# Kernel tuning notes

Hardware: AMD Instinct MI355X
Metric: run time of the kernel (lower is better)

Reference implementation:

```python
import jax, jax.numpy as jnp
import numpy as np

S = 1024          # tokens (prefill)
DIM = 2560
HEAD_DIM = 128
N_HEADS = 20
N_KV = 5
HPG = N_HEADS // N_KV      # heads per kv group = 4
GS = 128                   # weight-scale group size
THETA = 500000.0
EPS = 1e-05
QKV_OUT = (N_HEADS + 2 * N_KV) * HEAD_DIM  # 3840


def setup_inputs() -> dict:
    key = jax.random.key(0)
    ks = jax.random.split(key, 7)
    x = jax.random.normal(ks[0], (S, DIM), jnp.float32)
    # unpacked int2 (ternary) weights, stored as float for the reference math
    w_qkv = jax.random.randint(ks[1], (QKV_OUT, DIM), -1, 2).astype(jnp.float32)
    ws_qkv = jax.random.uniform(ks[2], (QKV_OUT, DIM // GS), jnp.float32, 0.01, 0.05)
    w_o = jax.random.randint(ks[3], (DIM, N_HEADS * HEAD_DIM), -1, 2).astype(jnp.float32)
    ws_o = jax.random.uniform(ks[4], (DIM, N_HEADS * HEAD_DIM // GS), jnp.float32, 0.01, 0.05)
    q_norm_w = 1.0 + 0.02 * jax.random.normal(ks[5], (HEAD_DIM,), jnp.float32)
    k_norm_w = 1.0 + 0.02 * jax.random.normal(ks[6], (HEAD_DIM,), jnp.float32)
    return {"x": x, "w_qkv": w_qkv, "ws_qkv": ws_qkv, "w_o": w_o, "ws_o": ws_o,
            "q_norm_w": q_norm_w, "k_norm_w": k_norm_w}


def _quant_act(x):
    # per-token symmetric int8 quant: s = 127 / max|x| (clamped)
    s = 127.0 / jnp.clip(jnp.max(jnp.abs(x), axis=-1, keepdims=True), 1e-05, None)
    q = jnp.clip(jnp.round(x * s), -128.0, 127.0)
    return q, s


def _bitlinear(x, w, ws):
    # int8 activation x int2 weight GEMM with per-(out,group) dequant scales
    q, s = _quant_act(x)
    w_dq = w * jnp.repeat(ws, GS, axis=1)        # [out, in]
    return (q @ w_dq.T) / s


def _rmsnorm(x, w):
    return x * jax.lax.rsqrt(jnp.mean(x * x, axis=-1, keepdims=True) + EPS) * w


def _rope(x, cos, sin):
    # x: [S, ..., d]; cos/sin: [S, d//2], interleaved-pair (llama) convention
    d2 = x.shape[-1] // 2
    shape = (x.shape[0],) + (1,) * (x.ndim - 2) + (d2,)
    c = cos.reshape(shape)
    s = sin.reshape(shape)
    xr = x.reshape(x.shape[:-1] + (d2, 2))
    x0, x1 = xr[..., 0], xr[..., 1]
    out = jnp.stack([x0 * c - x1 * s, x0 * s + x1 * c], axis=-1)
    return out.reshape(x.shape)


def reference(x, w_qkv, ws_qkv, w_o, ws_o, q_norm_w, k_norm_w):
    qkv = _bitlinear(x, w_qkv, ws_qkv)                       # [S, 3840]
    q_size = N_HEADS * HEAD_DIM
    k_size = N_KV * HEAD_DIM
    xq = qkv[:, :q_size].reshape(S, N_KV, HPG, HEAD_DIM)     # [S, g, h, d]
    xk = qkv[:, q_size:q_size + k_size].reshape(S, N_KV, HEAD_DIM)
    xv = qkv[:, q_size + k_size:].reshape(S, N_KV, HEAD_DIM)
    xq = _rmsnorm(xq, q_norm_w)
    xk = _rmsnorm(xk, k_norm_w)
    # RoPE (prefill: positions 0..S-1)
    pos = jnp.arange(S, dtype=jnp.float32)
    inv_freq = THETA ** (-jnp.arange(0, HEAD_DIM, 2, dtype=jnp.float32) / HEAD_DIM)
    ang = pos[:, None] * inv_freq[None, :]                   # [S, d/2]
    cos, sin = jnp.cos(ang), jnp.sin(ang)
    xq = _rope(xq, cos, sin)
    xk = _rope(xk, cos, sin)
    # GQA causal flash-attention math
    scale = HEAD_DIM ** -0.5
    scores = jnp.einsum('sghd,tgd->ghst', xq, xk) * scale    # [g, h, S, S]
    causal = jnp.tril(jnp.ones((S, S), bool))
    scores = jnp.where(causal, scores, -1e30)
    attn = jax.nn.softmax(scores, axis=-1)
    out = jnp.einsum('ghst,tgd->sghd', attn, xv).reshape(S, N_HEADS * HEAD_DIM)
    return _bitlinear(out, w_o, ws_o)                        # [S, DIM]
```

## Files before the change

### kernel.cpp

```cpp
#include <hip/hip_runtime.h>
#include <hip/hip_bf16.h>
#include <cstdint>
#include <math.h>

#define SEQ 1024
#define DIM 2560
#define HD 128
#define NH 20
#define NKV 5
#define QKV_OUT 3840
#define GS 128

typedef __bf16 bf16;
typedef __bf16 bf16x4 __attribute__((ext_vector_type(4)));
typedef __bf16 bf16x8 __attribute__((ext_vector_type(8)));
typedef float f32x4 __attribute__((ext_vector_type(4)));

template <typename T>
__global__ __launch_bounds__(256) void quant_kernel(
    const T* __restrict__ x, bf16* __restrict__ act,
    float* __restrict__ rs, int cols) {
  const int row = blockIdx.x;
  const int tid = threadIdx.x;
  const T* xr = x + (size_t)row * cols;
  float m = 0.f;
  for (int i = tid; i < cols; i += 256) m = fmaxf(m, fabsf((float)xr[i]));
  for (int off = 32; off; off >>= 1) m = fmaxf(m, __shfl_xor(m, off));
  __shared__ float red[4];
  __shared__ float s_bc;
  if ((tid & 63) == 0) red[tid >> 6] = m;
  __syncthreads();
  if (tid == 0) {
    float mm = fmaxf(fmaxf(red[0], red[1]), fmaxf(red[2], red[3]));
    mm = fmaxf(mm, 1e-5f);
    s_bc = 127.f / mm;
    rs[row] = mm / 127.f;
  }
  __syncthreads();
  const float s = s_bc;
  bf16* ar = act + (size_t)row * cols;
  for (int i = tid; i < cols; i += 256) {
    float q = rintf((float)xr[i] * s);
    q = fminf(fmaxf(q, -128.f), 127.f);
    ar[i] = (bf16)q;
  }
}

__global__ __launch_bounds__(256) void dequant2_kernel(
    const float* __restrict__ w1, const float* __restrict__ ws1, bf16* __restrict__ o1,
    const float* __restrict__ w2, const float* __restrict__ ws2, bf16* __restrict__ o2,
    long n1_4, long total4) {
  long i = (long)blockIdx.x * 256 + threadIdx.x;
  if (i >= total4) return;
  const float* w; const float* ws; bf16* o; long e;
  if (i < n1_4) { w = w1; ws = ws1; o = o1; e = i * 4; }
  else          { w = w2; ws = ws2; o = o2; e = (i - n1_4) * 4; }
  int row = (int)(e / DIM);
  int k = (int)(e % DIM);
  float sc = ws[(size_t)row * (DIM / GS) + (k / GS)];
  float4 wv = *(const float4*)(w + e);
  bf16x4 ov;
  ov[0] = (bf16)(wv.x * sc);
  ov[1] = (bf16)(wv.y * sc);
  ov[2] = (bf16)(wv.z * sc);
  ov[3] = (bf16)(wv.w * sc);
  *(bf16x4*)(o + e) = ov;
}

__device__ __forceinline__ void gload_lds16(const bf16* g, bf16* l) {
  __builtin_amdgcn_global_load_lds(
      (const __attribute__((address_space(1))) void*)g,
      (__attribute__((address_space(3))) void*)l, 16, 0, 0);
}

__global__ __launch_bounds__(256) void gemm_bt(
    const bf16* __restrict__ A, const bf16* __restrict__ B,
    const float* __restrict__ rs, float* __restrict__ C,
    int N, int K, int Kh, size_t part_stride) {
  __shared__ bf16 As[64 * 64];
  __shared__ bf16 Bs[128 * 64];
  const int tid = threadIdx.x;
  const int w = tid >> 6, l = tid & 63;
  const int row0 = blockIdx.y * 64;
  const int col0 = blockIdx.x * 128;
  const int z = blockIdx.z;
  const int wm = (w >> 1) * 32, wn = (w & 1) * 64;
  const int lcol = l & 15, quad = l >> 4;
  const int sr = l >> 3;
  const int sg = l & 7;
  const bf16* Ag = A + (size_t)row0 * K + (size_t)z * Kh;
  const bf16* Bg = B + (size_t)col0 * K + (size_t)z * Kh;

  f32x4 acc[2][4] = {};

  for (int k0 = 0; k0 < Kh; k0 += 64) {
    __syncthreads();
#pragma unroll
    for (int i = 0; i < 2; ++i) {
      int rb = w * 16 + i * 8;
      int r = rb + sr;
      gload_lds16(Ag + (size_t)r * K + k0 + ((sg ^ (r & 7)) * 8), As + rb * 64);
    }
#pragma unroll
    for (int i = 0; i < 4; ++i) {
      int rb = w * 32 + i * 8;
      int r = rb + sr;
      gload_lds16(Bg + (size_t)r * K + k0 + ((sg ^ (r & 7)) * 8), Bs + rb * 64);
    }
    __syncthreads();
#pragma unroll
    for (int ks = 0; ks < 2; ++ks) {
      bf16x8 af[2], bff[4];
#pragma unroll
      for (int mi = 0; mi < 2; ++mi) {
        int R = wm + mi * 16 + lcol;
        af[mi] = *(const bf16x8*)(As + R * 64 + (((ks * 4 + quad) ^ (R & 7)) * 8));
      }
#pragma unroll
      for (int ni = 0; ni < 4; ++ni) {
        int R = wn + ni * 16 + lcol;
        bff[ni] = *(const bf16x8*)(Bs + R * 64 + (((ks * 4 + quad) ^ (R & 7)) * 8));
      }
#pragma unroll
      for (int mi = 0; mi < 2; ++mi)
#pragma unroll
        for (int ni = 0; ni < 4; ++ni)
          acc[mi][ni] = __builtin_amdgcn_mfma_f32_16x16x32_bf16(
              af[mi], bff[ni], acc[mi][ni], 0, 0, 0);
    }
  }
  float* Cp = C + (size_t)z * part_stride;
#pragma unroll
  for (int mi = 0; mi < 2; ++mi) {
#pragma unroll
    for (int ni = 0; ni < 4; ++ni) {
      int col = col0 + wn + ni * 16 + lcol;
#pragma unroll
      for (int r = 0; r < 4; ++r) {
        int row = row0 + wm + mi * 16 + quad * 4 + r;
        Cp[(size_t)row * N + col] = acc[mi][ni][r] * rs[row];
      }
    }
  }
}

__global__ __launch_bounds__(256) void gemm_bt64(
    const bf16* __restrict__ A, const bf16* __restrict__ B,
    const float* __restrict__ rs, float* __restrict__ C, int N, int K) {
  __shared__ bf16 As[64 * 64];
  __shared__ bf16 Bs[64 * 64];
  const int tid = threadIdx.x;
  const int w = tid >> 6, l = tid & 63;
  const int row0 = blockIdx.y * 64;
  const int col0 = blockIdx.x * 64;
  const int wm = (w >> 1) * 32, wn = (w & 1) * 32;
  const int lcol = l & 15, quad = l >> 4;
  const int sr = l >> 3;
  const int sg = l & 7;
  const bf16* Ag = A + (size_t)row0 * K;
  const bf16* Bg = B + (size_t)col0 * K;

  f32x4 acc[2][2] = {};

  for (int k0 = 0; k0 < K; k0 += 64) {
    __syncthreads();
#pragma unroll
    for (int i = 0; i < 2; ++i) {
      int rb = w * 16 + i * 8;
      int r = rb + sr;
      gload_lds16(Ag + (size_t)r * K + k0 + ((sg ^ (r & 7)) * 8), As + rb * 64);
    }
#pragma unroll
    for (int i = 0; i < 2; ++i) {
      int rb = w * 16 + i * 8;
      int r = rb + sr;
      gload_lds16(Bg + (size_t)r * K + k0 + ((sg ^ (r & 7)) * 8), Bs + rb * 64);
    }
    __syncthreads();
#pragma unroll
    for (int ks = 0; ks < 2; ++ks) {
      bf16x8 af[2], bff[2];
#pragma unroll
      for (int mi = 0; mi < 2; ++mi) {
        int R = wm + mi * 16 + lcol;
        af[mi] = *(const bf16x8*)(As + R * 64 + (((ks * 4 + quad) ^ (R & 7)) * 8));
      }
#pragma unroll
      for (int ni = 0; ni < 2; ++ni) {
        int R = wn + ni * 16 + lcol;
        bff[ni] = *(const bf16x8*)(Bs + R * 64 + (((ks * 4 + quad) ^ (R & 7)) * 8));
      }
#pragma unroll
      for (int mi = 0; mi < 2; ++mi)
#pragma unroll
        for (int ni = 0; ni < 2; ++ni)
          acc[mi][ni] = __builtin_amdgcn_mfma_f32_16x16x32_bf16(
              af[mi], bff[ni], acc[mi][ni], 0, 0, 0);
    }
  }
#pragma unroll
  for (int mi = 0; mi < 2; ++mi) {
#pragma unroll
    for (int ni = 0; ni < 2; ++ni) {
      int col = col0 + wn + ni * 16 + lcol;
#pragma unroll
      for (int r = 0; r < 4; ++r) {
        int row = row0 + wm + mi * 16 + quad * 4 + r;
        C[(size_t)row * N + col] = acc[mi][ni][r] * rs[row];
      }
    }
  }
}

__global__ void qk_post(const float* __restrict__ qkvA, const float* __restrict__ qkvB,
                        const float* __restrict__ qw, const float* __restrict__ kw,
                        bf16* __restrict__ Qo, bf16* __restrict__ Ko) {
  const int t = blockIdx.x, h = blockIdx.y, i = threadIdx.x;
  const size_t off = (h < NH)
      ? (size_t)t * QKV_OUT + h * HD
      : (size_t)t * QKV_OUT + 2560 + (h - NH) * HD;
  const float* s1 = qkvA + off;
  const float* s2 = qkvB + off;
  float x0 = s1[2 * i] + s2[2 * i];
  float x1 = s1[2 * i + 1] + s2[2 * i + 1];
  float ss = x0 * x0 + x1 * x1;
  for (int off2 = 1; off2 < 64; off2 <<= 1) ss += __shfl_xor(ss, off2);
  float r = rsqrtf(ss * (1.f / 128.f) + 1e-5f);
  const float* wv = (h < NH) ? qw : kw;
  float y0 = x0 * r * wv[2 * i];
  float y1 = x1 * r * wv[2 * i + 1];
  float inv_freq = powf(500000.f, -(float)(2 * i) * (1.f / 128.f));
  float ang = (float)t * inv_freq;
  float sn, cs;
  sincosf(ang, &sn, &cs);
  float o0 = y0 * cs - y1 * sn;
  float o1 = y0 * sn + y1 * cs;
  if (h < NH) {
    bf16* dst = Qo + ((size_t)t * NH + h) * HD + 2 * i;
    dst[0] = (bf16)o0; dst[1] = (bf16)o1;
  } else {
    bf16* dst = Ko + ((size_t)(h - NH) * SEQ + t) * HD + 2 * i;
    dst[0] = (bf16)o0; dst[1] = (bf16)o1;
  }
}

__global__ __launch_bounds__(256) void v_post(const float* __restrict__ qkvA,
                                              const float* __restrict__ qkvB,
                                              bf16* __restrict__ Vt) {
  const int t0 = blockIdx.x * 64, g = blockIdx.y;
  const int tid = threadIdx.x;
  __shared__ bf16 Ls[64 * 137];
  {
    const int tl = tid >> 4;
    const int d0 = (tid & 15) * 8;
#pragma unroll
    for (int pass = 0; pass < 4; ++pass) {
      int t = pass * 16 + tl;
      size_t off = (size_t)(t0 + t) * QKV_OUT + 3200 + g * HD + d0;
      float4 a = *(const float4*)(qkvA + off);
      float4 b = *(const float4*)(qkvA + off + 4);
      float4 a2 = *(const float4*)(qkvB + off);
      float4 b2 = *(const float4*)(qkvB + off + 4);
      bf16* dst = Ls + t * 137 + d0;
      dst[0] = (bf16)(a.x + a2.x); dst[1] = (bf16)(a.y + a2.y);
      dst[2] = (bf16)(a.z + a2.z); dst[3] = (bf16)(a.w + a2.w);
      dst[4] = (bf16)(b.x + b2.x); dst[5] = (bf16)(b.y + b2.y);
      dst[6] = (bf16)(b.z + b2.z); dst[7] = (bf16)(b.w + b2.w);
    }
  }
  __syncthreads();
  {
    const int dl = tid >> 3;
    const int tl0 = (tid & 7) * 8;
#pragma unroll
    for (int pass = 0; pass < 4; ++pass) {
      int d = pass * 32 + dl;
      bf16x8 v;
#pragma unroll
      for (int j = 0; j < 8; ++j) v[j] = Ls[(tl0 + j) * 137 + d];
      *(bf16x8*)(Vt + ((size_t)g * HD + d) * SEQ + t0 + tl0) = v;
    }
  }
}

__global__ __launch_bounds__(256) void attn_mfma(
    const bf16* __restrict__ Qb, const bf16* __restrict__ Kb,
    const bf16* __restrict__ Vt, bf16* __restrict__ O) {
  const int qb = 31 - (int)blockIdx.x;
  const int hp = blockIdx.y;
  const int tid = threadIdx.x;
  const int wave = tid >> 6, lane = tid & 63;
  const int H = (hp >> 1) * 4 + (hp & 1) * 2 + (wave >> 1);
  const int g = H >> 2;
  const int qcol = lane & 15, quad = lane >> 4;
  const int q_tok = qb * 32 + (wave & 1) * 16 + qcol;
  const float scale = 0.08838834764831843f;

  __shared__ bf16 Ks[2][64 * 128];
  __shared__ bf16 Vs[2][128 * 64];

  const bf16* kbase = Kb + (size_t)g * SEQ * HD;
  const bf16* vbase = Vt + (size_t)g * HD * SEQ;

  bf16x8 qf[4];
  {
    const bf16* qp = Qb + ((size_t)q_tok * NH + H) * HD + quad * 8;
#pragma unroll
    for (int kc = 0; kc < 4; ++kc) qf[kc] = *(const bf16x8*)(qp + kc * 32);
  }

  float m_i = -1e30f, l_i = 0.f;
  f32x4 o_acc[8] = {};
  const int kt_max = (qb * 32 + 31) >> 6;

  const int k_r = lane >> 4, k_g = lane & 15;
  const int v_r = lane >> 3, v_g = lane & 7;

#define STAGE(buf, key0)                                                       \
  {                                                                            \
    _Pragma("unroll") for (int p = 0; p < 4; ++p) {                            \
      int r0 = wave * 16 + p * 4;                                              \
      int r = r0 + k_r;                                                        \
      gload_lds16(kbase + (size_t)((key0) + r) * HD + ((k_g ^ (r & 15)) * 8),  \
                  &Ks[buf][r0 * 128]);                                         \
    }                                                                          \
    _Pragma("unroll") for (int p = 0; p < 4; ++p) {                            \
      int r0 = wave * 32 + p * 8;                                              \
      int r = r0 + v_r;                                                        \
      gload_lds16(vbase + (size_t)r * SEQ + (key0) + ((v_g ^ (r & 7)) * 8),    \
                  &Vs[buf][r0 * 64]);                                          \
    }                                                                          \
  }

  STAGE(0, 0)

  for (int kt = 0; kt <= kt_max; ++kt) {
    const int key0 = kt * 64;
    __syncthreads();
    if (kt < kt_max) STAGE((kt + 1) & 1, key0 + 64)
    const bf16* Kt = Ks[kt & 1];
    const bf16* Vtile = Vs[kt & 1];

    f32x4 s[4];
#pragma unroll
    for (int mg = 0; mg < 4; ++mg) {
      const int R = mg * 16 + qcol;
      const bf16* krow = Kt + R * 128;
      f32x4 acc = {0.f, 0.f, 0.f, 0.f};
#pragma unroll
      for (int kc = 0; kc < 4; ++kc) {
        int j = kc * 4 + quad;
        bf16x8 kf = *(const bf16x8*)(krow + ((j ^ (R & 15)) * 8));
        acc = __builtin_amdgcn_mfma_f32_16x16x32_bf16(kf, qf[kc], acc, 0, 0, 0);
      }
      s[mg] = acc;
    }

    float mt = -1e30f;
#pragma unroll
    for (int mg = 0; mg < 4; ++mg)
#pragma unroll
      for (int r = 0; r < 4; ++r) {
        int key = key0 + mg * 16 + quad * 4 + r;
        float v = (key <= q_tok) ? s[mg][r] * scale : -1e30f;
        s[mg][r] = v;
        mt = fmaxf(mt, v);
      }
    mt = fmaxf(mt, __shfl_xor(mt, 16));
    mt = fmaxf(mt, __shfl_xor(mt, 32));
    float mnew = fmaxf(m_i, mt);
    float alpha = __expf(m_i - mnew);
    float ps = 0.f;
#pragma unroll
    for (int mg = 0; mg < 4; ++mg)
#pragma unroll
      for (int r = 0; r < 4; ++r) {
        float pv = __expf(s[mg][r] - mnew);
        s[mg][r] = pv;
        ps += pv;
      }
    ps += __shfl_xor(ps, 16);
    ps += __shfl_xor(ps, 32);
    l_i = l_i * alpha + ps;
    m_i = mnew;
#pragma unroll
    for (int mg2 = 0; mg2 < 8; ++mg2)
#pragma unroll
      for (int r = 0; r < 4; ++r) o_acc[mg2][r] *= alpha;

    bf16x8 pb[2];
#pragma unroll
    for (int c = 0; c < 2; ++c)
#pragma unroll
      for (int j = 0; j < 8; ++j)
        pb[c][j] = (bf16)s[c * 2 + (j >> 2)][j & 3];

#pragma unroll
    for (int mg2 = 0; mg2 < 8; ++mg2) {
      const int R = mg2 * 16 + qcol;
      const bf16* vrow = Vtile + R * 64;
      f32x4 acc = o_acc[mg2];
#pragma unroll
      for (int c = 0; c < 2; ++c) {
        int g8a = c * 8 + quad;
        int g8b = c * 8 + 4 + quad;
        bf16x4 v0 = *(const bf16x4*)(vrow + ((g8a >> 1) ^ (R & 7)) * 8 + (g8a & 1) * 4);
        bf16x4 v1 = *(const bf16x4*)(vrow + ((g8b >> 1) ^ (R & 7)) * 8 + (g8b & 1) * 4);
        bf16x8 vfr;
#pragma unroll
        for (int j = 0; j < 4; ++j) { vfr[j] = v0[j]; vfr[j + 4] = v1[j]; }
        acc = __builtin_amdgcn_mfma_f32_16x16x32_bf16(vfr, pb[c], acc, 0, 0, 0);
      }
      o_acc[mg2] = acc;
    }
  }
#undef STAGE

  const float inv = 1.f / l_i;
  bf16* op = O + (size_t)q_tok * DIM + H * HD + quad * 4;
#pragma unroll
  for (int mg2 = 0; mg2 < 8; ++mg2) {
    bf16x4 vv;
    vv[0] = (bf16)(o_acc[mg2][0] * inv);
    vv[1] = (bf16)(o_acc[mg2][1] * inv);
    vv[2] = (bf16)(o_acc[mg2][2] * inv);
    vv[3] = (bf16)(o_acc[mg2][3] * inv);
    *(bf16x4*)(op + mg2 * 16) = vv;
  }
}

extern "C" void kernel_launch(void* const* d_in, const int* in_sizes, int n_in,
                              void* d_out, int out_size, void* d_ws, size_t ws_size,
                              hipStream_t stream) {
  const float* x      = (const float*)d_in[0];
  const float* w_qkv  = (const float*)d_in[1];
  const float* ws_qkv = (const float*)d_in[2];
  const float* w_o    = (const float*)d_in[3];
  const float* ws_o   = (const float*)d_in[4];
  const float* qnw    = (const float*)d_in[5];
  const float* knw    = (const float*)d_in[6];
  float* out = (float*)d_out;

  char* p = (char*)d_ws;
  bf16*  act1 = (bf16*)p;  p += (size_t)SEQ * DIM * 2;
  float* rs1  = (float*)p; p += 4096;
  bf16*  wqdq = (bf16*)p;  p += (size_t)QKV_OUT * DIM * 2;
  bf16*  wodq = (bf16*)p;  p += (size_t)DIM * DIM * 2;
  float* qkvA = (float*)p; p += (size_t)SEQ * QKV_OUT * 4;
  float* qkvB = (float*)p; p += (size_t)SEQ * QKV_OUT * 4;
  bf16*  Qb   = (bf16*)p;  p += (size_t)SEQ * NH * HD * 2;
  bf16*  Kb   = (bf16*)p;  p += (size_t)NKV * SEQ * HD * 2;
  bf16*  Vt   = (bf16*)p;  p += (size_t)NKV * HD * SEQ * 2;
  bf16*  attn = (bf16*)p;  p += (size_t)SEQ * DIM * 2;
  bf16*  act2 = (bf16*)p;  p += (size_t)SEQ * DIM * 2;
  float* rs2  = (float*)p; p += 4096;

  quant_kernel<float><<<SEQ, 256, 0, stream>>>(x, act1, rs1, DIM);
  {
    long n1_4 = (long)QKV_OUT * DIM / 4;
    long total4 = n1_4 + (long)DIM * DIM / 4;
    dequant2_kernel<<<(int)((total4 + 255) / 256), 256, 0, stream>>>(
        w_qkv, ws_qkv, wqdq, w_o, ws_o, wodq, n1_4, total4);
  }
  gemm_bt<<<dim3(QKV_OUT / 128, SEQ / 64, 2), 256, 0, stream>>>(
      act1, wqdq, rs1, qkvA, QKV_OUT, DIM, DIM / 2, (size_t)SEQ * QKV_OUT);
  qk_post<<<dim3(SEQ, 25), 64, 0, stream>>>(qkvA, qkvB, qnw, knw, Qb, Kb);
  v_post<<<dim3(SEQ / 64, NKV), 256, 0, stream>>>(qkvA, qkvB, Vt);
  attn_mfma<<<dim3(32, 10), 256, 0, stream>>>(Qb, Kb, Vt, attn);
  quant_kernel<bf16><<<SEQ, 256, 0, stream>>>(attn, act2, rs2, DIM);
  gemm_bt64<<<dim3(DIM / 64, SEQ / 64), 256, 0, stream>>>(
      act2, wodq, rs2, out, DIM, DIM);
}
```

Before: 242.9 us.

## Fuse weight dequantization into GEMM loads and double-buffer the K loop

The separate weight-dequant kernel and its bf16 weight buffers are removed. A templated GEMM now reads the fp32 ternary weights and group scales directly, scales and converts them to bf16 in registers, and writes them into swizzled shared memory. The K loop is double-buffered so the next tile's loads overlap the current MFMA work. This drops one kernel launch and a full write-then-read of the dequantized weights. In exchange, each row-block re-reads fp32 weights (twice the bytes of bf16) and repeats the conversion work, and register pressure goes up.

```diff
diff --git a/kernel.cpp b/kernel.cpp
--- a/kernel.cpp
+++ b/kernel.cpp
@@ -46,167 +46,127 @@
   }
 }
 
-__global__ __launch_bounds__(256) void dequant2_kernel(
-    const float* __restrict__ w1, const float* __restrict__ ws1, bf16* __restrict__ o1,
-    const float* __restrict__ w2, const float* __restrict__ ws2, bf16* __restrict__ o2,
-    long n1_4, long total4) {
-  long i = (long)blockIdx.x * 256 + threadIdx.x;
-  if (i >= total4) return;
-  const float* w; const float* ws; bf16* o; long e;
-  if (i < n1_4) { w = w1; ws = ws1; o = o1; e = i * 4; }
-  else          { w = w2; ws = ws2; o = o2; e = (i - n1_4) * 4; }
-  int row = (int)(e / DIM);
-  int k = (int)(e % DIM);
-  float sc = ws[(size_t)row * (DIM / GS) + (k / GS)];
-  float4 wv = *(const float4*)(w + e);
-  bf16x4 ov;
-  ov[0] = (bf16)(wv.x * sc);
-  ov[1] = (bf16)(wv.y * sc);
-  ov[2] = (bf16)(wv.z * sc);
-  ov[3] = (bf16)(wv.w * sc);
-  *(bf16x4*)(o + e) = ov;
-}
-
 __device__ __forceinline__ void gload_lds16(const bf16* g, bf16* l) {
   __builtin_amdgcn_global_load_lds(
       (const __attribute__((address_space(1))) void*)g,
       (__attribute__((address_space(3))) void*)l, 16, 0, 0);
 }
 
-__global__ __launch_bounds__(256) void gemm_bt(
-    const bf16* __restrict__ A, const bf16* __restrict__ B,
-    const float* __restrict__ rs, float* __restrict__ C,
-    int N, int K, int Kh, size_t part_stride) {
-  __shared__ bf16 As[64 * 64];
-  __shared__ bf16 Bs[128 * 64];
+template <int BN>
+__global__ __launch_bounds__(256) void gemm_fused(
+    const bf16* __restrict__ A, const float* __restrict__ W,
+    const float* __restrict__ WS, const float* __restrict__ rs,
+    float* __restrict__ C, int N, int K, int Kh, size_t part_stride) {
+  constexpr int NW = BN / 32;
+  constexpr int NPASS = BN * 8 / 256;
+  __shared__ bf16 As[2][64 * 64];
+  __shared__ bf16 Bs[2][BN * 64];
   const int tid = threadIdx.x;
   const int w = tid >> 6, l = tid & 63;
   const int row0 = blockIdx.y * 64;
-  const int col0 = blockIdx.x * 128;
+  const int col0 = blockIdx.x * BN;
   const int z = blockIdx.z;
-  const int wm = (w >> 1) * 32, wn = (w & 1) * 64;
+  const int wm = (w >> 1) * 32, wn = (w & 1) * (BN / 2);
   const int lcol = l & 15, quad = l >> 4;
-  const int sr = l >> 3;
-  const int sg = l & 7;
+  const int sr = l >> 3, sg = l & 7;
   const bf16* Ag = A + (size_t)row0 * K + (size_t)z * Kh;
-  const bf16* Bg = B + (size_t)col0 * K + (size_t)z * Kh;
-
-  f32x4 acc[2][4] = {};
-
+  const int ksc = K / GS;
+
+  int brow[NPASS], bj[NPASS];
+#pragma unroll
+  for (int p = 0; p < NPASS; ++p) {
+    int gI = p * 256 + tid;
+    brow[p] = gI >> 3;
+    bj[p] = gI & 7;
+  }
+
+  float4 bl[NPASS][2];
+  float bsc[NPASS];
+  f32x4 acc[2][NW] = {};
+
+#define STAGE_A(buf, k0)                                                       \
+  {                                                                            \
+    _Pragma("unroll") for (int i = 0; i < 2; ++i) {                            \
+      int rb = w * 16 + i * 8;                                                 \
+      int r = rb + sr;                                                         \
+      gload_lds16(Ag + (size_t)r * K + (k0) + ((sg ^ (r & 7)) * 8),            \
+                  &As[buf][rb * 64]);                                          \
+    }                                                                          \
+  }
+#define LOAD_B(k0)                                                             \
+  {                                                                            \
+    int grp = (z * Kh + (k0)) / GS;                                            \
+    _Pragma("unroll") for (int p = 0; p < NPASS; ++p) {                        \
+      const float* wp =                                                        \
+          W + (size_t)(col0 + brow[p]) * K + (size_t)z * Kh + (k0) + bj[p] * 8;\
+      bl[p][0] = *(const float4*)wp;                                           \
+      bl[p][1] = *(const float4*)(wp + 4);                                     \
+      bsc[p] = WS[(size_t)(col0 + brow[p]) * ksc + grp];                       \
+    }                                                                          \
+  }
+#define WRITE_B(buf)                                                           \
+  {                                                                            \
+    _Pragma("unroll") for (int p = 0; p < NPASS; ++p) {                        \
+      float sc = bsc[p];                                                       \
+      bf16x8 o;                                                                \
+      o[0] = (bf16)(bl[p][0].x * sc); o[1] = (bf16)(bl[p][0].y * sc);          \
+      o[2] = (bf16)(bl[p][0].z * sc); o[3] = (bf16)(bl[p][0].w * sc);          \
+      o[4] = (bf16)(bl[p][1].x * sc); o[5] = (bf16)(bl[p][1].y * sc);          \
+      o[6] = (bf16)(bl[p][1].z * sc); o[7] = (bf16)(bl[p][1].w * sc);          \
+      *(bf16x8*)&Bs[buf][brow[p] * 64 + ((bj[p] ^ (brow[p] & 7)) * 8)] = o;    \
+    }                                                                          \
+  }
+
+  STAGE_A(0, 0)
+  LOAD_B(0)
+  WRITE_B(0)
+  __syncthreads();
+
+  int buf = 0;
   for (int k0 = 0; k0 < Kh; k0 += 64) {
-    __syncthreads();
-#pragma unroll
-    for (int i = 0; i < 2; ++i) {
-      int rb = w * 16 + i * 8;
-      int r = rb + sr;
-      gload_lds16(Ag + (size_t)r * K + k0 + ((sg ^ (r & 7)) * 8), As + rb * 64);
-    }
-#pragma unroll
-    for (int i = 0; i < 4; ++i) {
-      int rb = w * 32 + i * 8;
-      int r = rb + sr;
-      gload_lds16(Bg + (size_t)r * K + k0 + ((sg ^ (r & 7)) * 8), Bs + rb * 64);
-    }
-    __syncthreads();
+    const bool has_next = (k0 + 64) < Kh;
+    if (has_next) {
+      STAGE_A(buf ^ 1, k0 + 64)
+      LOAD_B(k0 + 64)
+    }
 #pragma unroll
     for (int ks = 0; ks < 2; ++ks) {
-      bf16x8 af[2], bff[4];
+      bf16x8 af[2], bff[NW];
 #pragma unroll
       for (int mi = 0; mi < 2; ++mi) {
         int R = wm + mi * 16 + lcol;
-        af[mi] = *(const bf16x8*)(As + R * 64 + (((ks * 4 + quad) ^ (R & 7)) * 8));
-      }
-#pragma unroll
-      for (int ni = 0; ni < 4; ++ni) {
+        af[mi] = *(const bf16x8*)(&As[buf][R * 64 + (((ks * 4 + quad) ^ (R & 7)) * 8)]);
+      }
+#pragma unroll
+      for (int ni = 0; ni < NW; ++ni) {
         int R = wn + ni * 16 + lcol;
-        bff[ni] = *(const bf16x8*)(Bs + R * 64 + (((ks * 4 + quad) ^ (R & 7)) * 8));
+        bff[ni] = *(const bf16x8*)(&Bs[buf][R * 64 + (((ks * 4 + quad) ^ (R & 7)) * 8)]);
       }
 #pragma unroll
       for (int mi = 0; mi < 2; ++mi)
 #pragma unroll
-        for (int ni = 0; ni < 4; ++ni)
+        for (int ni = 0; ni < NW; ++ni)
           acc[mi][ni] = __builtin_amdgcn_mfma_f32_16x16x32_bf16(
               af[mi], bff[ni], acc[mi][ni], 0, 0, 0);
     }
-  }
+    if (has_next) WRITE_B(buf ^ 1)
+    __syncthreads();
+    buf ^= 1;
+  }
+#undef STAGE_A
+#undef LOAD_B
+#undef WRITE_B
+
   float* Cp = C + (size_t)z * part_stride;
 #pragma unroll
   for (int mi = 0; mi < 2; ++mi) {
 #pragma unroll
-    for (int ni = 0; ni < 4; ++ni) {
+    for (int ni = 0; ni < NW; ++ni) {
       int col = col0 + wn + ni * 16 + lcol;
 #pragma unroll
       for (int r = 0; r < 4; ++r) {
         int row = row0 + wm + mi * 16 + quad * 4 + r;
         Cp[(size_t)row * N + col] = acc[mi][ni][r] * rs[row];
-      }
-    }
-  }
-}
-
-__global__ __launch_bounds__(256) void gemm_bt64(
-    const bf16* __restrict__ A, const bf16* __restrict__ B,
-    const float* __restrict__ rs, float* __restrict__ C, int N, int K) {
-  __shared__ bf16 As[64 * 64];
-  __shared__ bf16 Bs[64 * 64];
-  const int tid = threadIdx.x;
-  const int w = tid >> 6, l = tid & 63;
-  const int row0 = blockIdx.y * 64;
-  const int col0 = blockIdx.x * 64;
-  const int wm = (w >> 1) * 32, wn = (w & 1) * 32;
-  const int lcol = l & 15, quad = l >> 4;
-  const int sr = l >> 3;
-  const int sg = l & 7;
-  const bf16* Ag = A + (size_t)row0 * K;
-  const bf16* Bg = B + (size_t)col0 * K;
-
-  f32x4 acc[2][2] = {};
-
-  for (int k0 = 0; k0 < K; k0 += 64) {
-    __syncthreads();
-#pragma unroll
-    for (int i = 0; i < 2; ++i) {
-      int rb = w * 16 + i * 8;
-      int r = rb + sr;
-      gload_lds16(Ag + (size_t)r * K + k0 + ((sg ^ (r & 7)) * 8), As + rb * 64);
-    }
-#pragma unroll
-    for (int i = 0; i < 2; ++i) {
-      int rb = w * 16 + i * 8;
-      int r = rb + sr;
-      gload_lds16(Bg + (size_t)r * K + k0 + ((sg ^ (r & 7)) * 8), Bs + rb * 64);
-    }
-    __syncthreads();
-#pragma unroll
-    for (int ks = 0; ks < 2; ++ks) {
-      bf16x8 af[2], bff[2];
-#pragma unroll
-      for (int mi = 0; mi < 2; ++mi) {
-        int R = wm + mi * 16 + lcol;
-        af[mi] = *(const bf16x8*)(As + R * 64 + (((ks * 4 + quad) ^ (R & 7)) * 8));
-      }
-#pragma unroll
-      for (int ni = 0; ni < 2; ++ni) {
-        int R = wn + ni * 16 + lcol;
-        bff[ni] = *(const bf16x8*)(Bs + R * 64 + (((ks * 4 + quad) ^ (R & 7)) * 8));
-      }
-#pragma unroll
-      for (int mi = 0; mi < 2; ++mi)
-#pragma unroll
-        for (int ni = 0; ni < 2; ++ni)
-          acc[mi][ni] = __builtin_amdgcn_mfma_f32_16x16x32_bf16(
-              af[mi], bff[ni], acc[mi][ni], 0, 0, 0);
-    }
-  }
-#pragma unroll
-  for (int mi = 0; mi < 2; ++mi) {
-#pragma unroll
-    for (int ni = 0; ni < 2; ++ni) {
-      int col = col0 + wn + ni * 16 + lcol;
-#pragma unroll
-      for (int r = 0; r < 4; ++r) {
-        int row = row0 + wm + mi * 16 + quad * 4 + r;
-        C[(size_t)row * N + col] = acc[mi][ni][r] * rs[row];
       }
     }
   }
@@ -444,8 +404,6 @@
   char* p = (char*)d_ws;
   bf16*  act1 = (bf16*)p;  p += (size_t)SEQ * DIM * 2;
   float* rs1  = (float*)p; p += 4096;
-  bf16*  wqdq = (bf16*)p;  p += (size_t)QKV_OUT * DIM * 2;
-  bf16*  wodq = (bf16*)p;  p += (size_t)DIM * DIM * 2;
   float* qkvA = (float*)p; p += (size_t)SEQ * QKV_OUT * 4;
   float* qkvB = (float*)p; p += (size_t)SEQ * QKV_OUT * 4;
   bf16*  Qb   = (bf16*)p;  p += (size_t)SEQ * NH * HD * 2;
@@ -456,18 +414,12 @@
   float* rs2  = (float*)p; p += 4096;
 
   quant_kernel<float><<<SEQ, 256, 0, stream>>>(x, act1, rs1, DIM);
-  {
-    long n1_4 = (long)QKV_OUT * DIM / 4;
-    long total4 = n1_4 + (long)DIM * DIM / 4;
-    dequant2_kernel<<<(int)((total4 + 255) / 256), 256, 0, stream>>>(
-        w_qkv, ws_qkv, wqdq, w_o, ws_o, wodq, n1_4, total4);
-  }
-  gemm_bt<<<dim3(QKV_OUT / 128, SEQ / 64, 2), 256, 0, stream>>>(
-      act1, wqdq, rs1, qkvA, QKV_OUT, DIM, DIM / 2, (size_t)SEQ * QKV_OUT);
+  gemm_fused<128><<<dim3(QKV_OUT / 128, SEQ / 64, 2), 256, 0, stream>>>(
+      act1, w_qkv, ws_qkv, rs1, qkvA, QKV_OUT, DIM, DIM / 2, (size_t)SEQ * QKV_OUT);
   qk_post<<<dim3(SEQ, 25), 64, 0, stream>>>(qkvA, qkvB, qnw, knw, Qb, Kb);
   v_post<<<dim3(SEQ / 64, NKV), 256, 0, stream>>>(qkvA, qkvB, Vt);
   attn_mfma<<<dim3(32, 10), 256, 0, stream>>>(Qb, Kb, Vt, attn);
   quant_kernel<bf16><<<SEQ, 256, 0, stream>>>(attn, act2, rs2, DIM);
-  gemm_bt64<<<dim3(DIM / 64, SEQ / 64), 256, 0, stream>>>(
-      act2, wodq, rs2, out, DIM, DIM);
-}
+  gemm_fused<64><<<dim3(DIM / 64, SEQ / 64, 1), 256, 0, stream>>>(
+      act2, w_o, ws_o, rs2, out, DIM, DIM, DIM, 0);
+}
```

Result: slower. 292.7 us (+20.5%).
